# Kernel tuning notes

Hardware: AMD Instinct MI355X
Metric: run time of the kernel (lower is better)

Reference implementation:

```python
import jax, jax.numpy as jnp
import numpy as np

# Static problem sizes (see shape_source)
B, SX, SY = 256, 256, 70          # graphs, encoder nodes/graph, decoder nodes/graph
F, EMB, H = 512, 256, 256          # f_size, emb_size, h_size
VOCAB = 256
E = 4 * B * SY                     # 71680 edges
N_SLT = 4                          # SltEdgeTypes
N_SRT = 8                          # len(SrtEdgeTypes)


def setup_inputs() -> dict:
    key = jax.random.key(0)
    ks = jax.random.split(key, 24)
    s = 0.02
    inp = {
        'x': jax.random.normal(ks[0], (B * SX, F), jnp.float32),
        'x_batch': jnp.repeat(jnp.arange(B, dtype=jnp.int64), SX),
        'tgt_y': jax.random.randint(ks[1], (B * SY,), 0, VOCAB, jnp.int64),
        'tgt_edge_index': jax.random.randint(ks[2], (2, E), 0, B * SY, jnp.int64),
        'tgt_edge_type': jax.random.randint(ks[3], (E,), 0, N_SLT, jnp.int64),
        'tgt_y_batch': jnp.repeat(jnp.arange(B, dtype=jnp.int64), SY),
        'embeds': jax.random.normal(ks[4], (VOCAB, EMB), jnp.float32) * s,
    }
    dims = [(EMB, H), (H, H), (H, EMB)]
    k = 5
    for l, (din, dout) in enumerate(dims, start=1):
        inp[f'W_in{l}'] = jax.random.normal(ks[k + 0], (din, dout), jnp.float32) * s
        inp[f'Wq{l}'] = jax.random.normal(ks[k + 1], (dout, F), jnp.float32) * s
        inp[f'Wv{l}'] = jax.random.normal(ks[k + 2], (F, dout), jnp.float32) * s
        inp[f'Ee{l}'] = jax.random.normal(ks[k + 3], (N_SLT, dout), jnp.float32) * s
        k += 4
    inp['lin_z_w'] = jax.random.normal(ks[k], (EMB, VOCAB), jnp.float32) * s
    inp['lin_z_b'] = jnp.zeros((VOCAB,), jnp.float32)
    inp['lin_g_w'] = jax.random.normal(ks[k + 1], (2 * EMB, N_SRT), jnp.float32) * s
    inp['lin_g_b'] = jnp.zeros((N_SRT,), jnp.float32)
    return inp


def gcn_dec_layer(x_b, y, src, tgt, etype, W_in, Wq, Wv, Ee):
    """Edge-type-conditioned message passing + cross-attention onto encoder x.
    x_b: [B,SX,F]; y: [Ny,din]. Returns ([Ny,dout], alpha [B,SY,SX])."""
    h = y @ W_in                                   # [Ny, dout]
    m = h[src] + Ee[etype]                         # gather + type embedding
    agg = jax.ops.segment_sum(m, tgt, num_segments=y.shape[0])
    q = (h @ Wq).reshape(B, SY, F)                 # query into encoder space
    logits = jnp.einsum('bqf,bkf->bqk', q, x_b) / jnp.sqrt(jnp.float32(F))
    alpha = jax.nn.softmax(logits, axis=-1)        # [B,SY,SX]
    ctx = jnp.einsum('bqk,bkf->bqf', alpha, x_b) @ Wv  # [B,SY,dout]
    out = jax.nn.relu(h + agg + ctx.reshape(h.shape[0], -1))
    return out, alpha


def reference(x, x_batch, tgt_y, tgt_edge_index, tgt_edge_type, tgt_y_batch,
              embeds, W_in1, Wq1, Wv1, Ee1, W_in2, Wq2, Wv2, Ee2,
              W_in3, Wq3, Wv3, Ee3, lin_z_w, lin_z_b, lin_g_w, lin_g_b):
    x_b = x.reshape(B, SX, F)
    src, tgt = tgt_edge_index[0], tgt_edge_index[1]
    y = embeds[tgt_y]                              # [Ny, EMB]
    y, a1 = gcn_dec_layer(x_b, y, src, tgt, tgt_edge_type, W_in1, Wq1, Wv1, Ee1)
    y, a2 = gcn_dec_layer(x_b, y, src, tgt, tgt_edge_type, W_in2, Wq2, Wv2, Ee2)
    y, a3 = gcn_dec_layer(x_b, y, src, tgt, tgt_edge_type, W_in3, Wq3, Wv3, Ee3)
    y_score = y @ lin_z_w + lin_z_b                # [Ny, VOCAB]
    ef = y[tgt_edge_index]                         # [2, E, EMB]
    ef = jnp.transpose(ef, (1, 0, 2)).reshape(E, 2 * EMB)
    y_edge_rel_score = ef @ lin_g_w + lin_g_b      # [E, N_SRT]
    return (y, y_score, y_edge_rel_score, a1, a2, a3)
```

## Files before the change

### kernel.cpp

```cpp
#include <hip/hip_runtime.h>
#include <cstddef>
#include <cstdint>

#define B_    256
#define SX_   256
#define SY_   70
#define F_    512
#define EMB_  256
#define NY_   (B_*SY_)
#define NE_   (4*B_*SY_)

typedef short s16x8 __attribute__((ext_vector_type(8)));
typedef float f32x4 __attribute__((ext_vector_type(4)));
typedef unsigned short us4 __attribute__((ext_vector_type(4)));
typedef unsigned short us8 __attribute__((ext_vector_type(8)));

__device__ __forceinline__ unsigned short f2bf(float f) {
    unsigned u = __builtin_bit_cast(unsigned, f);
    u += 0x7fffu + ((u >> 16) & 1u);
    return (unsigned short)(u >> 16);
}
__device__ __forceinline__ float bf2f(unsigned short b) {
    unsigned u = ((unsigned)b) << 16;
    return __builtin_bit_cast(float, u);
}

template<int EPI, int SWZ>
__global__ __launch_bounds__(256, 2)
void gemm_mfma(const unsigned short* __restrict__ A, int lda, long sAb,
               const unsigned short* __restrict__ Bt, int ldb, long sBb,
               float* __restrict__ Cf, int ldc, long sCfb,
               unsigned short* __restrict__ Cb, int ldcb, long sCbb,
               const float* __restrict__ aux1, long sAux,
               int M, int K, float scale, int nx, int ny)
{
    __shared__ unsigned short As[128 * 64];
    __shared__ unsigned short Bs[128 * 64];
    char* AsB = (char*)As;
    char* BsB = (char*)Bs;
    const int tid = threadIdx.x;
    int bxi, byi, z;
    if (SWZ) {
        const int nwg = gridDim.x;
        const int bid = blockIdx.x;
        const int wg = (bid & 7) * (nwg >> 3) + (bid >> 3);
        bxi = wg % nx;
        byi = (wg / nx) % ny;
        z   = wg / (nx * ny);
    } else {
        bxi = blockIdx.x; byi = blockIdx.y; z = blockIdx.z;
    }
    A  += (size_t)z * sAb;
    Bt += (size_t)z * sBb;
    const char* auxp = (const char*)aux1 + (size_t)z * sAux;
    const int bm = byi * 128, bn = bxi * 128;
    const int lane = tid & 63;
    const int w = tid >> 6, wr = w >> 1, wc = w & 1;
    const int l15 = lane & 15, lq = lane >> 4;

    f32x4 acc[4][4];
    const f32x4 z4 = {0.f, 0.f, 0.f, 0.f};
#pragma unroll
    for (int m = 0; m < 4; ++m)
#pragma unroll
        for (int n = 0; n < 4; ++n) acc[m][n] = z4;

    for (int k0 = 0; k0 < K; k0 += 64) {
#pragma unroll
        for (int i = 0; i < 4; ++i) {
            const int row = i * 32 + (tid >> 3);
            const int k8  = (tid & 7) ^ (row & 7);
            int ra = bm + row; ra = (ra < M) ? ra : (M - 1);
            const unsigned short* g = A + (size_t)ra * lda + k0 + k8 * 8;
            __builtin_amdgcn_global_load_lds(
                (const __attribute__((address_space(1))) unsigned int*)g,
                (__attribute__((address_space(3))) unsigned int*)(AsB + i * 4096 + tid * 16),
                16, 0, 0);
        }
#pragma unroll
        for (int i = 0; i < 4; ++i) {
            const int row = i * 32 + (tid >> 3);
            const int k8  = (tid & 7) ^ (row & 7);
            const unsigned short* g = Bt + (size_t)(bn + row) * ldb + k0 + k8 * 8;
            __builtin_amdgcn_global_load_lds(
                (const __attribute__((address_space(1))) unsigned int*)g,
                (__attribute__((address_space(3))) unsigned int*)(BsB + i * 4096 + tid * 16),
                16, 0, 0);
        }
        __syncthreads();
#pragma unroll
        for (int kk = 0; kk < 2; ++kk) {
            s16x8 af[4], bf[4];
#pragma unroll
            for (int m = 0; m < 4; ++m) {
                const int row = wr * 64 + m * 16 + l15;
                const int slot = (kk * 4 + lq) ^ (row & 7);
                af[m] = *(const s16x8*)(AsB + row * 128 + slot * 16);
            }
#pragma unroll
            for (int n = 0; n < 4; ++n) {
                const int col = wc * 64 + n * 16 + l15;
                const int slot = (kk * 4 + lq) ^ (col & 7);
                bf[n] = *(const s16x8*)(BsB + col * 128 + slot * 16);
            }
#pragma unroll
            for (int m = 0; m < 4; ++m)
#pragma unroll
                for (int n = 0; n < 4; ++n)
                    acc[m][n] = __builtin_amdgcn_mfma_f32_16x16x32_bf16(
                        af[m], bf[n], acc[m][n], 0, 0, 0);
        }
        __syncthreads();
    }

    float* cf = Cf ? Cf + (size_t)z * sCfb : nullptr;
    unsigned short* cb = Cb ? Cb + (size_t)z * sCbb : nullptr;
#pragma unroll
    for (int m = 0; m < 4; ++m) {
#pragma unroll
        for (int n = 0; n < 4; ++n) {
            const int col = bn + wc * 64 + n * 16 + l15;
            f32x4 v = acc[m][n];
#pragma unroll
            for (int r = 0; r < 4; ++r) {
                const int gr = bm + wr * 64 + m * 16 + lq * 4 + r;
                if (gr >= M) continue;
                float o = v[r] * scale;
                if (EPI == 4) o += ((const float*)auxp)[col];
                if (EPI == 7) {
                    if (col < 256) cb[(size_t)gr * ldcb + col] = f2bf(o);
                    else ((unsigned short*)cf)[(size_t)gr * 512 + (col - 256)] = f2bf(o);
                } else {
                    if (cf) cf[(size_t)gr * ldc + col] = o;
                    if (cb) cb[(size_t)gr * ldcb + col] = f2bf(o);
                }
            }
        }
    }
}

template<int LAST>
__global__ __launch_bounds__(512, 1)
void attn_pv(const unsigned short* __restrict__ Q,
             const unsigned short* __restrict__ X,
             const unsigned short* __restrict__ XV,
             long sXVb,
             const unsigned short* __restrict__ aggb,
             const unsigned short* __restrict__ lzT,
             const float* __restrict__ lzb,
             float* __restrict__ Aout,
             unsigned short* __restrict__ Yb,
             float* __restrict__ Yf,
             float* __restrict__ Score,
             float scale)
{
    __shared__ unsigned short As[128 * 64];
    __shared__ unsigned short Bs[256 * 64];
    __shared__ unsigned short Al[128 * 256];
    __shared__ float red[4][2][64];
    char* AsB = (char*)As;
    char* BsB = (char*)Bs;
    char* AlB = (char*)Al;
    const int tid = threadIdx.x;
    const int z = blockIdx.x;
    const unsigned short* Qb  = Q + (size_t)z * SY_ * F_;
    const unsigned short* Xb  = X + (size_t)z * SX_ * F_;
    const unsigned short* xvb = XV + (size_t)z * sXVb;
    const int lane = tid & 63;
    const int w = tid >> 6, wr = w >> 2, wc = w & 3;
    const int l15 = lane & 15, lq = lane >> 4;

    f32x4 acc[4][4];
    const f32x4 z4 = {0.f, 0.f, 0.f, 0.f};
#pragma unroll
    for (int m = 0; m < 4; ++m)
#pragma unroll
        for (int n = 0; n < 4; ++n) acc[m][n] = z4;

    for (int k0 = 0; k0 < F_; k0 += 64) {
#pragma unroll
        for (int i = 0; i < 2; ++i) {
            const int row = i * 64 + (tid >> 3);
            const int k8  = (tid & 7) ^ (row & 7);
            const int ra = (row < SY_) ? row : (SY_ - 1);
            const unsigned short* g = Qb + (size_t)ra * F_ + k0 + k8 * 8;
            __builtin_amdgcn_global_load_lds(
                (const __attribute__((address_space(1))) unsigned int*)g,
                (__attribute__((address_space(3))) unsigned int*)(AsB + i * 8192 + tid * 16),
                16, 0, 0);
        }
#pragma unroll
        for (int i = 0; i < 4; ++i) {
            const int row = i * 64 + (tid >> 3);
            const int k8  = (tid & 7) ^ (row & 7);
            const unsigned short* g = Xb + (size_t)row * F_ + k0 + k8 * 8;
            __builtin_amdgcn_global_load_lds(
                (const __attribute__((address_space(1))) unsigned int*)g,
                (__attribute__((address_space(3))) unsigned int*)(BsB + i * 8192 + tid * 16),
                16, 0, 0);
        }
        __syncthreads();
#pragma unroll
        for (int kk = 0; kk < 2; ++kk) {
            s16x8 af[4], bf[4];
#pragma unroll
            for (int m = 0; m < 4; ++m) {
                const int row = wr * 64 + m * 16 + l15;
                const int slot = (kk * 4 + lq) ^ (row & 7);
                af[m] = *(const s16x8*)(AsB + row * 128 + slot * 16);
            }
#pragma unroll
            for (int n = 0; n < 4; ++n) {
                const int col = wc * 64 + n * 16 + l15;
                const int slot = (kk * 4 + lq) ^ (col & 7);
                bf[n] = *(const s16x8*)(BsB + col * 128 + slot * 16);
            }
#pragma unroll
            for (int m = 0; m < 4; ++m)
#pragma unroll
                for (int n = 0; n < 4; ++n)
                    acc[m][n] = __builtin_amdgcn_mfma_f32_16x16x32_bf16(
                        af[m], bf[n], acc[m][n], 0, 0, 0);
        }
        __syncthreads();
    }

#pragma unroll
    for (int m = 0; m < 4; ++m)
#pragma unroll
        for (int n = 0; n < 4; ++n)
#pragma unroll
            for (int r = 0; r < 4; ++r) acc[m][n][r] *= scale;

    float rmax[4][4];
#pragma unroll
    for (int m = 0; m < 4; ++m)
#pragma unroll
        for (int r = 0; r < 4; ++r) {
            float mx = acc[m][0][r];
#pragma unroll
            for (int n = 1; n < 4; ++n) mx = fmaxf(mx, acc[m][n][r]);
            mx = fmaxf(mx, __shfl_xor(mx, 1));
            mx = fmaxf(mx, __shfl_xor(mx, 2));
            mx = fmaxf(mx, __shfl_xor(mx, 4));
            mx = fmaxf(mx, __shfl_xor(mx, 8));
            rmax[m][r] = mx;
        }
    if (l15 == 0) {
#pragma unroll
        for (int m = 0; m < 4; ++m)
#pragma unroll
            for (int r = 0; r < 4; ++r)
                red[wc][wr][m * 16 + lq * 4 + r] = rmax[m][r];
    }
    __syncthreads();
    float rtot[4][4];
#pragma unroll
    for (int m = 0; m < 4; ++m)
#pragma unroll
        for (int r = 0; r < 4; ++r) {
            const int lr = m * 16 + lq * 4 + r;
            rtot[m][r] = fmaxf(fmaxf(red[0][wr][lr], red[1][wr][lr]),
                               fmaxf(red[2][wr][lr], red[3][wr][lr]));
        }
    __syncthreads();
    float rsum[4][4];
#pragma unroll
    for (int m = 0; m < 4; ++m)
#pragma unroll
        for (int r = 0; r < 4; ++r) {
            float s = 0.f;
#pragma unroll
            for (int n = 0; n < 4; ++n) {
                float e = __expf(acc[m][n][r] - rtot[m][r]);
                acc[m][n][r] = e;
                s += e;
            }
            s += __shfl_xor(s, 1);
            s += __shfl_xor(s, 2);
            s += __shfl_xor(s, 4);
            s += __shfl_xor(s, 8);
            rsum[m][r] = s;
        }
    if (l15 == 0) {
#pragma unroll
        for (int m = 0; m < 4; ++m)
#pragma unroll
            for (int r = 0; r < 4; ++r)
                red[wc][wr][m * 16 + lq * 4 + r] = rsum[m][r];
    }
    __syncthreads();
    float* ao = Aout + (size_t)z * SY_ * SX_;
#pragma unroll
    for (int m = 0; m < 4; ++m)
#pragma unroll
        for (int r = 0; r < 4; ++r) {
            const int lr = m * 16 + lq * 4 + r;
            const int row = wr * 64 + lr;
            const float inv = 1.0f / (red[0][wr][lr] + red[1][wr][lr] +
                                      red[2][wr][lr] + red[3][wr][lr]);
#pragma unroll
            for (int n = 0; n < 4; ++n) {
                const int col = wc * 64 + n * 16 + l15;
                const float o = acc[m][n][r] * inv;
                if (row < SY_) ao[(size_t)row * SX_ + col] = o;
                *(unsigned short*)(AlB + row * 512 +
                    (((col >> 3) ^ (row & 7)) << 4) + ((col & 7) << 1)) = f2bf(o);
            }
        }
    __syncthreads();

    f32x4 oac[4][4];
#pragma unroll
    for (int m = 0; m < 4; ++m)
#pragma unroll
        for (int n = 0; n < 4; ++n) oac[m][n] = z4;

    for (int ks = 0; ks < 4; ++ks) {
        const int k0 = ks * 64;
#pragma unroll
        for (int i = 0; i < 4; ++i) {
            const int row = i * 64 + (tid >> 3);
            const int k8  = (tid & 7) ^ (row & 7);
            const unsigned short* g = xvb + (size_t)row * 256 + k0 + k8 * 8;
            __builtin_amdgcn_global_load_lds(
                (const __attribute__((address_space(1))) unsigned int*)g,
                (__attribute__((address_space(3))) unsigned int*)(BsB + i * 8192 + tid * 16),
                16, 0, 0);
        }
        __syncthreads();
#pragma unroll
        for (int kk = 0; kk < 2; ++kk) {
            s16x8 af[4], bf[4];
#pragma unroll
            for (int m = 0; m < 4; ++m) {
                const int row = wr * 64 + m * 16 + l15;
                const int chunk = (k0 >> 3) + kk * 4 + lq;
                af[m] = *(const s16x8*)(AlB + row * 512 + ((chunk ^ (row & 7)) << 4));
            }
#pragma unroll
            for (int n = 0; n < 4; ++n) {
                const int col = wc * 64 + n * 16 + l15;
                const int slot = (kk * 4 + lq) ^ (col & 7);
                bf[n] = *(const s16x8*)(BsB + col * 128 + slot * 16);
            }
#pragma unroll
            for (int m = 0; m < 4; ++m)
#pragma unroll
                for (int n = 0; n < 4; ++n)
                    oac[m][n] = __builtin_amdgcn_mfma_f32_16x16x32_bf16(
                        af[m], bf[n], oac[m][n], 0, 0, 0);
        }
        __syncthreads();
    }

#pragma unroll
    for (int m = 0; m < 4; ++m)
#pragma unroll
        for (int n = 0; n < 4; ++n) {
            const int col = wc * 64 + n * 16 + l15;
            f32x4 v = oac[m][n];
#pragma unroll
            for (int r = 0; r < 4; ++r) {
                const int row = wr * 64 + m * 16 + lq * 4 + r;
                if (row >= SY_) continue;
                const size_t node = (size_t)z * SY_ + row;
                float o = v[r] + bf2f(aggb[node * 256 + col]);
                o = fmaxf(o, 0.f);
                const unsigned short ob = f2bf(o);
                Yb[node * 256 + col] = ob;
                if (Yf) Yf[node * 256 + col] = o;
                if (LAST)
                    *(unsigned short*)(AlB + row * 512 +
                        (((col >> 3) ^ (row & 7)) << 4) + ((col & 7) << 1)) = ob;
            }
        }

    if (LAST) {
        __syncthreads();
#pragma unroll
        for (int m = 0; m < 4; ++m)
#pragma unroll
            for (int n = 0; n < 4; ++n) oac[m][n] = z4;
        for (int ks = 0; ks < 4; ++ks) {
            const int k0 = ks * 64;
#pragma unroll
            for (int i = 0; i < 4; ++i) {
                const int row = i * 64 + (tid >> 3);
                const int k8  = (tid & 7) ^ (row & 7);
                const unsigned short* g = lzT + (size_t)row * 256 + k0 + k8 * 8;
                __builtin_amdgcn_global_load_lds(
                    (const __attribute__((address_space(1))) unsigned int*)g,
                    (__attribute__((address_space(3))) unsigned int*)(BsB + i * 8192 + tid * 16),
                    16, 0, 0);
            }
            __syncthreads();
#pragma unroll
            for (int kk = 0; kk < 2; ++kk) {
                s16x8 af[4], bf[4];
#pragma unroll
                for (int m = 0; m < 4; ++m) {
                    const int row = wr * 64 + m * 16 + l15;
                    const int chunk = (k0 >> 3) + kk * 4 + lq;
                    af[m] = *(const s16x8*)(AlB + row * 512 + ((chunk ^ (row & 7)) << 4));
                }
#pragma unroll
                for (int n = 0; n < 4; ++n) {
                    const int col = wc * 64 + n * 16 + l15;
                    const int slot = (kk * 4 + lq) ^ (col & 7);
                    bf[n] = *(const s16x8*)(BsB + col * 128 + slot * 16);
                }
#pragma unroll
                for (int m = 0; m < 4; ++m)
#pragma unroll
                    for (int n = 0; n < 4; ++n)
                        oac[m][n] = __builtin_amdgcn_mfma_f32_16x16x32_bf16(
                            af[m], bf[n], oac[m][n], 0, 0, 0);
            }
            __syncthreads();
        }
#pragma unroll
        for (int m = 0; m < 4; ++m)
#pragma unroll
            for (int n = 0; n < 4; ++n) {
                const int col = wc * 64 + n * 16 + l15;
                f32x4 v = oac[m][n];
#pragma unroll
                for (int r = 0; r < 4; ++r) {
                    const int row = wr * 64 + m * 16 + lq * 4 + r;
                    if (row >= SY_) continue;
                    Score[((size_t)z * SY_ + row) * 256 + col] = v[r] + lzb[col];
                }
            }
    }
}

__global__ __launch_bounds__(256)
void conv_x(const float* __restrict__ in, unsigned short* __restrict__ out, int n8)
{
    for (int i = blockIdx.x * 256 + threadIdx.x; i < n8; i += 2048 * 256) {
        float4 a = ((const float4*)in)[i * 2];
        float4 b = ((const float4*)in)[i * 2 + 1];
        us8 o = { f2bf(a.x), f2bf(a.y), f2bf(a.z), f2bf(a.w),
                  f2bf(b.x), f2bf(b.y), f2bf(b.z), f2bf(b.w) };
        ((us8*)out)[i] = o;
    }
}

struct WAll {
    const float* src[10];
    unsigned short* dst[10];
    int R[10];
    int C[10];
};

__global__ __launch_bounds__(256)
void conv_wT_all(WAll d)
{
    const int z = blockIdx.z;
    const int R = d.R[z], C = d.C[z];
    const int c0 = blockIdx.x * 64, r0 = blockIdx.y * 64;
    if (c0 >= C || r0 >= R) return;
    const float* in = d.src[z];
    unsigned short* outT = d.dst[z];
    __shared__ unsigned short t[64][65];
    const int r = threadIdx.x >> 4, cq = (threadIdx.x & 15) << 2;
#pragma unroll
    for (int i = 0; i < 4; ++i) {
        const int rr = r + i * 16;
        float4 v = *(const float4*)(in + (size_t)(r0 + rr) * C + c0 + cq);
        t[rr][cq + 0] = f2bf(v.x); t[rr][cq + 1] = f2bf(v.y);
        t[rr][cq + 2] = f2bf(v.z); t[rr][cq + 3] = f2bf(v.w);
    }
    __syncthreads();
    const int c = threadIdx.x >> 2, sq = (threadIdx.x & 3) << 4;
    us8 o0, o1;
#pragma unroll
    for (int i = 0; i < 8; ++i) { o0[i] = t[sq + i][c]; o1[i] = t[sq + 8 + i][c]; }
    *(us8*)(outT + (size_t)(c0 + c) * R + r0 + sq) = o0;
    *(us8*)(outT + (size_t)(c0 + c) * R + r0 + sq + 8) = o1;
}

__global__ __launch_bounds__(256)
void gather_embed(const float* __restrict__ embeds, const int* __restrict__ tgt_y,
                  unsigned short* __restrict__ yb)
{
    const int i = blockIdx.x * 8 + (threadIdx.x >> 5);
    const int c8 = (threadIdx.x & 31) * 8;
    const int v = tgt_y[i];
    const float* p = embeds + (size_t)v * 256 + c8;
    float4 a = *(const float4*)p;
    float4 b = *(const float4*)(p + 4);
    us8 o = { f2bf(a.x), f2bf(a.y), f2bf(a.z), f2bf(a.w),
              f2bf(b.x), f2bf(b.y), f2bf(b.z), f2bf(b.w) };
    *(us8*)(yb + (size_t)i * 256 + c8) = o;
}

__global__ __launch_bounds__(256)
void edge_deg(const int* __restrict__ tgt, int* __restrict__ deg)
{
    const int e = blockIdx.x * 256 + threadIdx.x;
    if (e < NE_) atomicAdd(&deg[tgt[e]], 1);
}

__global__ __launch_bounds__(1024)
void scan_off(const int* __restrict__ deg, int* __restrict__ off, int* __restrict__ cursor)
{
    __shared__ int ls[1024];
    const int t = threadIdx.x;
    const int base = t * 18;
    int local[18];
    int s = 0;
#pragma unroll
    for (int i = 0; i < 18; ++i) {
        const int idx = base + i;
        const int v = (idx < NY_) ? deg[idx] : 0;
        local[i] = s; s += v;
    }
    ls[t] = s;
    __syncthreads();
    for (int d = 1; d < 1024; d <<= 1) {
        int v = (t >= d) ? ls[t - d] : 0;
        __syncthreads();
        ls[t] += v;
        __syncthreads();
    }
    const int excl = (t == 0) ? 0 : ls[t - 1];
#pragma unroll
    for (int i = 0; i < 18; ++i) {
        const int idx = base + i;
        if (idx < NY_) {
            const int o = excl + local[i];
            off[idx] = o; cursor[idx] = o;
        }
    }
    if (t == 1023) off[NY_] = ls[1023];
}

__global__ __launch_bounds__(256)
void edge_fill(const int* __restrict__ tgt, int* __restrict__ cursor,
               int* __restrict__ elist)
{
    const int e = blockIdx.x * 256 + threadIdx.x;
    if (e >= NE_) return;
    const int pos = atomicAdd(&cursor[tgt[e]], 1);
    elist[pos] = e;
}

__global__ __launch_bounds__(256)
void node_agg(const unsigned short* __restrict__ hb,
              const float* __restrict__ Ee,
              const int* __restrict__ src, const int* __restrict__ etype,
              const int* __restrict__ off, const int* __restrict__ elist,
              unsigned short* __restrict__ aggb)
{
    const int nid  = blockIdx.x * 4 + (threadIdx.x >> 6);
    const int lane = threadIdx.x & 63;
    const int c = lane * 4;
    const int k0 = off[nid], k1 = off[nid + 1];
    us4 sv = *(const us4*)(hb + (size_t)nid * 256 + c);
    float4 acc;
    acc.x = bf2f(sv[0]); acc.y = bf2f(sv[1]);
    acc.z = bf2f(sv[2]); acc.w = bf2f(sv[3]);
    int cnt0 = 0, cnt1 = 0, cnt2 = 0, cnt3 = 0;
    for (int k = k0; k < k1; ++k) {
        const int e = elist[k];
        const int sfrom = src[e];
        const int ty = etype[e];
        us4 hv = *(const us4*)(hb + (size_t)sfrom * 256 + c);
        acc.x += bf2f(hv[0]); acc.y += bf2f(hv[1]);
        acc.z += bf2f(hv[2]); acc.w += bf2f(hv[3]);
        cnt0 += (ty == 0); cnt1 += (ty == 1); cnt2 += (ty == 2); cnt3 += (ty == 3);
    }
    float4 e0 = *(const float4*)(Ee + c);
    float4 e1 = *(const float4*)(Ee + 256 + c);
    float4 e2 = *(const float4*)(Ee + 512 + c);
    float4 e3 = *(const float4*)(Ee + 768 + c);
    acc.x += cnt0 * e0.x + cnt1 * e1.x + cnt2 * e2.x + cnt3 * e3.x;
    acc.y += cnt0 * e0.y + cnt1 * e1.y + cnt2 * e2.y + cnt3 * e3.y;
    acc.z += cnt0 * e0.z + cnt1 * e1.z + cnt2 * e2.z + cnt3 * e3.z;
    acc.w += cnt0 * e0.w + cnt1 * e1.w + cnt2 * e2.w + cnt3 * e3.w;
    us4 o = { f2bf(acc.x), f2bf(acc.y), f2bf(acc.z), f2bf(acc.w) };
    *(us4*)(aggb + (size_t)nid * 256 + c) = o;
}

__global__ __launch_bounds__(256)
void edge_w(const float* __restrict__ y, const float* __restrict__ W,
            float* __restrict__ Y12)
{
    __shared__ float Ws[4096];
    __shared__ float ys[16][260];
    const int tid = threadIdx.x;
#pragma unroll
    for (int i = 0; i < 4; ++i)
        ((float4*)Ws)[i * 256 + tid] = ((const float4*)W)[i * 256 + tid];
    const int r = tid >> 4, seg = tid & 15;
    const int r0 = blockIdx.x * 16;
#pragma unroll
    for (int i = 0; i < 4; ++i) {
        const int c4 = seg + i * 16;
        *(float4*)&ys[r][c4 * 4] = *(const float4*)(y + (size_t)(r0 + r) * 256 + c4 * 4);
    }
    __syncthreads();
    const int j = tid & 15;
    const int row = tid >> 4;
    const float* Wcol = Ws + ((j < 8) ? j : (2048 + j - 8));
    float acc = 0.f;
#pragma unroll 4
    for (int c = 0; c < 256; ++c) acc = fmaf(ys[row][c], Wcol[c * 8], acc);
    Y12[(size_t)(r0 + row) * 16 + j] = acc;
}

__global__ __launch_bounds__(256)
void edge_gather(const float* __restrict__ Y12, const int* __restrict__ src,
                 const int* __restrict__ tgt, const float* __restrict__ bias,
                 float* __restrict__ esc)
{
    const int e = blockIdx.x * 256 + threadIdx.x;
    if (e >= NE_) return;
    const float* a = Y12 + (size_t)src[e] * 16;
    const float* b = Y12 + (size_t)tgt[e] * 16 + 8;
    float4 a0 = ((const float4*)a)[0], a1 = ((const float4*)a)[1];
    float4 b0 = ((const float4*)b)[0], b1 = ((const float4*)b)[1];
    float4 c0 = ((const float4*)bias)[0], c1 = ((const float4*)bias)[1];
    float4 o0, o1;
    o0.x = a0.x + b0.x + c0.x; o0.y = a0.y + b0.y + c0.y;
    o0.z = a0.z + b0.z + c0.z; o0.w = a0.w + b0.w + c0.w;
    o1.x = a1.x + b1.x + c1.x; o1.y = a1.y + b1.y + c1.y;
    o1.z = a1.z + b1.z + c1.z; o1.w = a1.w + b1.w + c1.w;
    ((float4*)(esc + (size_t)e * 8))[0] = o0;
    ((float4*)(esc + (size_t)e * 8))[1] = o1;
}

extern "C" void kernel_launch(void* const* d_in, const int* in_sizes, int n_in,
                              void* d_out, int out_size, void* d_ws, size_t ws_size,
                              hipStream_t stream)
{
    const float* x       = (const float*)d_in[0];
    const int*   tgt_y   = (const int*)d_in[2];
    const int*   eidx    = (const int*)d_in[3];
    const int*   etype   = (const int*)d_in[4];
    const float* embeds  = (const float*)d_in[6];
    const float* W_in[3] = {(const float*)d_in[7],  (const float*)d_in[11], (const float*)d_in[15]};
    const float* Wq[3]   = {(const float*)d_in[8],  (const float*)d_in[12], (const float*)d_in[16]};
    const float* Wv[3]   = {(const float*)d_in[9],  (const float*)d_in[13], (const float*)d_in[17]};
    const float* Ee[3]   = {(const float*)d_in[10], (const float*)d_in[14], (const float*)d_in[18]};
    const float* lin_z_w = (const float*)d_in[19];
    const float* lin_z_b = (const float*)d_in[20];
    const float* lin_g_w = (const float*)d_in[21];
    const float* lin_g_b = (const float*)d_in[22];
    const int* src = eidx;
    const int* tgt = eidx + NE_;

    float* out = (float*)d_out;
    float* y_final = out;
    float* score   = out + 4587520;
    float* esc     = out + 9175040;
    float* aout[3] = {out + 9748480, out + 14336000, out + 18923520};

    char* wsb = (char*)d_ws;
    unsigned short* xb     = (unsigned short*)(wsb + 0);
    unsigned short* xvTall = (unsigned short*)(wsb + 67108864);
    unsigned short* hb     = (unsigned short*)(wsb + 167772160);
    unsigned short* aggb   = (unsigned short*)(wsb + 176947200);
    unsigned short* qb     = (unsigned short*)(wsb + 186122240);
    unsigned short* yb     = (unsigned short*)(wsb + 204472320);
    char* wt = wsb + 213647360;
    unsigned short* wcatT[3], *wqT[3], *wvT[3];
    for (int l = 0; l < 3; ++l) {
        wcatT[l] = (unsigned short*)(wt + l * 393216);
        wqT[l]   = (unsigned short*)(wt + 1179648 + l * 262144);
        wvT[l]   = (unsigned short*)(wt + 1966080 + l * 262144);
    }
    unsigned short* lzT = (unsigned short*)(wt + 2752512);
    char* extra = wsb + 216530944;
    float* Y12    = (float*)extra;
    int*   deg    = (int*)(extra + 1146880);
    int*   off    = (int*)(extra + 1218560);
    int*   cursor = (int*)(extra + 1290244);
    int*   elist  = (int*)(extra + 1361924);

    hipMemsetAsync(deg, 0, NY_ * sizeof(int), stream);
    edge_deg<<<280, 256, 0, stream>>>(tgt, deg);
    scan_off<<<1, 1024, 0, stream>>>(deg, off, cursor);
    edge_fill<<<280, 256, 0, stream>>>(tgt, cursor, elist);

    conv_x<<<2048, 256, 0, stream>>>(x, xb, 4194304);
    WAll wd;
    for (int l = 0; l < 3; ++l) {
        wd.src[l]     = W_in[l]; wd.dst[l]     = wcatT[l]; wd.R[l]     = 256; wd.C[l]     = 256;
        wd.src[3 + l] = Wq[l];   wd.dst[3 + l] = wqT[l];   wd.R[3 + l] = 256; wd.C[3 + l] = 512;
        wd.src[6 + l] = Wv[l];   wd.dst[6 + l] = wvT[l];   wd.R[6 + l] = 512; wd.C[6 + l] = 256;
    }
    wd.src[9] = lin_z_w; wd.dst[9] = lzT; wd.R[9] = 256; wd.C[9] = 256;
    conv_wT_all<<<dim3(8, 8, 10), 256, 0, stream>>>(wd);
    gather_embed<<<2240, 256, 0, stream>>>(embeds, tgt_y, yb);

    gemm_mfma<0, 0><<<dim3(2, 4, 3), 256, 0, stream>>>(
        wqT[0], 256, 131072L,  wcatT[0], 256, 196608L,
        nullptr, 0, 0,  wcatT[0] + 65536, 256, 196608L,
        nullptr, 0, 512, 256, 1.f, 0, 0);

    gemm_mfma<0, 1><<<3072, 256, 0, stream>>>(
        wvT[0], 512, 0,  xb, 512, (long)SX_ * F_,
        nullptr, 0, 0,  xvTall, 256, 768L * 256,
        nullptr, 0, 768, 512, 1.f, 2, 6);

    const float qscale = 0.044194173824159216f;
    for (int l = 0; l < 3; ++l) {
        gemm_mfma<7, 0><<<dim3(6, 140, 1), 256, 0, stream>>>(
            yb, 256, 0,  wcatT[l], 256, 0,
            (float*)qb, 512, 0,  hb, 256, 0,
            nullptr, 0, NY_, 256, 1.f, 0, 0);
        node_agg<<<4480, 256, 0, stream>>>(hb, Ee[l], src, etype, off, elist, aggb);
        if (l < 2) {
            attn_pv<0><<<256, 512, 0, stream>>>(
                qb, xb, xvTall + (size_t)l * 65536, 768L * 256,
                aggb, nullptr, nullptr,
                aout[l], yb, nullptr, nullptr, qscale);
        } else {
            attn_pv<1><<<256, 512, 0, stream>>>(
                qb, xb, xvTall + (size_t)l * 65536, 768L * 256,
                aggb, lzT, lin_z_b,
                aout[l], yb, y_final, score, qscale);
        }
    }
    edge_w<<<1120, 256, 0, stream>>>(y_final, lin_g_w, Y12);
    edge_gather<<<280, 256, 0, stream>>>(Y12, src, tgt, lin_g_b, esc);
}
```

Baseline: 444.7 us.

## Fuse CSR build into one kernel, merge embed gather, fold edge_w into attention

Collapses the memset, degree count, scan and fill into a single one-block kernel using LDS atomics. Merges the embedding gather into the x conversion launch. Moves the per-node edge-weight projection into the last attention kernel, reading the final y from LDS. This cuts launch count and a y reload, but the single-block CSR build serialises 71680 edges on one CU, and the fused epilogue runs scalar FMA loops at the tail of attn_pv.

```diff
diff --git a/kernel.cpp b/kernel.cpp
--- a/kernel.cpp
+++ b/kernel.cpp
@@ -148,6 +148,8 @@
              const unsigned short* __restrict__ aggb,
              const unsigned short* __restrict__ lzT,
              const float* __restrict__ lzb,
+             const float* __restrict__ gw,
+             float* __restrict__ Y12g,
              float* __restrict__ Aout,
              unsigned short* __restrict__ Yb,
              float* __restrict__ Yf,
@@ -432,18 +434,49 @@
                     Score[((size_t)z * SY_ + row) * 256 + col] = v[r] + lzb[col];
                 }
             }
+
+        __syncthreads();
+        float* Ws = (float*)BsB;
+        for (int i = tid; i < 1024; i += 512)
+            ((float4*)Ws)[i] = ((const float4*)gw)[i];
+        __syncthreads();
+        for (int t = tid; t < 1120; t += 512) {
+            const int row = t >> 4, j = t & 15;
+            const float* Wcol = Ws + ((j < 8) ? j : (2048 + j - 8));
+            float a2 = 0.f;
+            for (int c = 0; c < 256; ++c) {
+                const float yv = bf2f(*(const unsigned short*)(AlB + row * 512 +
+                    (((c >> 3) ^ (row & 7)) << 4) + ((c & 7) << 1)));
+                a2 = fmaf(yv, Wcol[c * 8], a2);
+            }
+            Y12g[((size_t)z * SY_ + row) * 16 + j] = a2;
+        }
     }
 }
 
 __global__ __launch_bounds__(256)
-void conv_x(const float* __restrict__ in, unsigned short* __restrict__ out, int n8)
+void conv_x_embed(const float* __restrict__ in, unsigned short* __restrict__ out,
+                  int n8, const float* __restrict__ embeds,
+                  const int* __restrict__ tgt_y, unsigned short* __restrict__ yb)
 {
-    for (int i = blockIdx.x * 256 + threadIdx.x; i < n8; i += 2048 * 256) {
-        float4 a = ((const float4*)in)[i * 2];
-        float4 b = ((const float4*)in)[i * 2 + 1];
+    if (blockIdx.x < 2048) {
+        for (int i = blockIdx.x * 256 + threadIdx.x; i < n8; i += 2048 * 256) {
+            float4 a = ((const float4*)in)[i * 2];
+            float4 b = ((const float4*)in)[i * 2 + 1];
+            us8 o = { f2bf(a.x), f2bf(a.y), f2bf(a.z), f2bf(a.w),
+                      f2bf(b.x), f2bf(b.y), f2bf(b.z), f2bf(b.w) };
+            ((us8*)out)[i] = o;
+        }
+    } else {
+        const int i = (blockIdx.x - 2048) * 8 + (threadIdx.x >> 5);
+        const int c8 = (threadIdx.x & 31) * 8;
+        const int v = tgt_y[i];
+        const float* p = embeds + (size_t)v * 256 + c8;
+        float4 a = *(const float4*)p;
+        float4 b = *(const float4*)(p + 4);
         us8 o = { f2bf(a.x), f2bf(a.y), f2bf(a.z), f2bf(a.w),
                   f2bf(b.x), f2bf(b.y), f2bf(b.z), f2bf(b.w) };
-        ((us8*)out)[i] = o;
+        *(us8*)(yb + (size_t)i * 256 + c8) = o;
     }
 }
 
@@ -481,40 +514,24 @@
     *(us8*)(outT + (size_t)(c0 + c) * R + r0 + sq + 8) = o1;
 }
 
-__global__ __launch_bounds__(256)
-void gather_embed(const float* __restrict__ embeds, const int* __restrict__ tgt_y,
-                  unsigned short* __restrict__ yb)
+__global__ __launch_bounds__(1024)
+void build_csr(const int* __restrict__ tgt, int* __restrict__ off,
+               int* __restrict__ elist)
 {
-    const int i = blockIdx.x * 8 + (threadIdx.x >> 5);
-    const int c8 = (threadIdx.x & 31) * 8;
-    const int v = tgt_y[i];
-    const float* p = embeds + (size_t)v * 256 + c8;
-    float4 a = *(const float4*)p;
-    float4 b = *(const float4*)(p + 4);
-    us8 o = { f2bf(a.x), f2bf(a.y), f2bf(a.z), f2bf(a.w),
-              f2bf(b.x), f2bf(b.y), f2bf(b.z), f2bf(b.w) };
-    *(us8*)(yb + (size_t)i * 256 + c8) = o;
-}
-
-__global__ __launch_bounds__(256)
-void edge_deg(const int* __restrict__ tgt, int* __restrict__ deg)
-{
-    const int e = blockIdx.x * 256 + threadIdx.x;
-    if (e < NE_) atomicAdd(&deg[tgt[e]], 1);
-}
-
-__global__ __launch_bounds__(1024)
-void scan_off(const int* __restrict__ deg, int* __restrict__ off, int* __restrict__ cursor)
-{
+    __shared__ int ldeg[NY_];
     __shared__ int ls[1024];
     const int t = threadIdx.x;
+    for (int i = t; i < NY_; i += 1024) ldeg[i] = 0;
+    __syncthreads();
+    for (int e = t; e < NE_; e += 1024) atomicAdd(&ldeg[tgt[e]], 1);
+    __syncthreads();
     const int base = t * 18;
     int local[18];
     int s = 0;
 #pragma unroll
     for (int i = 0; i < 18; ++i) {
         const int idx = base + i;
-        const int v = (idx < NY_) ? deg[idx] : 0;
+        const int v = (idx < NY_) ? ldeg[idx] : 0;
         local[i] = s; s += v;
     }
     ls[t] = s;
@@ -531,20 +548,16 @@
         const int idx = base + i;
         if (idx < NY_) {
             const int o = excl + local[i];
-            off[idx] = o; cursor[idx] = o;
+            off[idx] = o;
+            ldeg[idx] = o;
         }
     }
     if (t == 1023) off[NY_] = ls[1023];
-}
-
-__global__ __launch_bounds__(256)
-void edge_fill(const int* __restrict__ tgt, int* __restrict__ cursor,
-               int* __restrict__ elist)
-{
-    const int e = blockIdx.x * 256 + threadIdx.x;
-    if (e >= NE_) return;
-    const int pos = atomicAdd(&cursor[tgt[e]], 1);
-    elist[pos] = e;
+    __syncthreads();
+    for (int e = t; e < NE_; e += 1024) {
+        const int pos = atomicAdd(&ldeg[tgt[e]], 1);
+        elist[pos] = e;
+    }
 }
 
 __global__ __launch_bounds__(256)
@@ -585,33 +598,6 @@
 }
 
 __global__ __launch_bounds__(256)
-void edge_w(const float* __restrict__ y, const float* __restrict__ W,
-            float* __restrict__ Y12)
-{
-    __shared__ float Ws[4096];
-    __shared__ float ys[16][260];
-    const int tid = threadIdx.x;
-#pragma unroll
-    for (int i = 0; i < 4; ++i)
-        ((float4*)Ws)[i * 256 + tid] = ((const float4*)W)[i * 256 + tid];
-    const int r = tid >> 4, seg = tid & 15;
-    const int r0 = blockIdx.x * 16;
-#pragma unroll
-    for (int i = 0; i < 4; ++i) {
-        const int c4 = seg + i * 16;
-        *(float4*)&ys[r][c4 * 4] = *(const float4*)(y + (size_t)(r0 + r) * 256 + c4 * 4);
-    }
-    __syncthreads();
-    const int j = tid & 15;
-    const int row = tid >> 4;
-    const float* Wcol = Ws + ((j < 8) ? j : (2048 + j - 8));
-    float acc = 0.f;
-#pragma unroll 4
-    for (int c = 0; c < 256; ++c) acc = fmaf(ys[row][c], Wcol[c * 8], acc);
-    Y12[(size_t)(r0 + row) * 16 + j] = acc;
-}
-
-__global__ __launch_bounds__(256)
 void edge_gather(const float* __restrict__ Y12, const int* __restrict__ src,
                  const int* __restrict__ tgt, const float* __restrict__ bias,
                  float* __restrict__ esc)
@@ -675,17 +661,12 @@
     unsigned short* lzT = (unsigned short*)(wt + 2752512);
     char* extra = wsb + 216530944;
     float* Y12    = (float*)extra;
-    int*   deg    = (int*)(extra + 1146880);
-    int*   off    = (int*)(extra + 1218560);
-    int*   cursor = (int*)(extra + 1290244);
-    int*   elist  = (int*)(extra + 1361924);
-
-    hipMemsetAsync(deg, 0, NY_ * sizeof(int), stream);
-    edge_deg<<<280, 256, 0, stream>>>(tgt, deg);
-    scan_off<<<1, 1024, 0, stream>>>(deg, off, cursor);
-    edge_fill<<<280, 256, 0, stream>>>(tgt, cursor, elist);
-
-    conv_x<<<2048, 256, 0, stream>>>(x, xb, 4194304);
+    int*   off    = (int*)(extra + 1146880);
+    int*   elist  = (int*)(extra + 1218568);
+
+    build_csr<<<1, 1024, 0, stream>>>(tgt, off, elist);
+
+    conv_x_embed<<<4288, 256, 0, stream>>>(x, xb, 4194304, embeds, tgt_y, yb);
     WAll wd;
     for (int l = 0; l < 3; ++l) {
         wd.src[l]     = W_in[l]; wd.dst[l]     = wcatT[l]; wd.R[l]     = 256; wd.C[l]     = 256;
@@ -694,7 +675,6 @@
     }
     wd.src[9] = lin_z_w; wd.dst[9] = lzT; wd.R[9] = 256; wd.C[9] = 256;
     conv_wT_all<<<dim3(8, 8, 10), 256, 0, stream>>>(wd);
-    gather_embed<<<2240, 256, 0, stream>>>(embeds, tgt_y, yb);
 
     gemm_mfma<0, 0><<<dim3(2, 4, 3), 256, 0, stream>>>(
         wqT[0], 256, 131072L,  wcatT[0], 256, 196608L,
@@ -716,15 +696,14 @@
         if (l < 2) {
             attn_pv<0><<<256, 512, 0, stream>>>(
                 qb, xb, xvTall + (size_t)l * 65536, 768L * 256,
-                aggb, nullptr, nullptr,
+                aggb, nullptr, nullptr, nullptr, nullptr,
                 aout[l], yb, nullptr, nullptr, qscale);
         } else {
             attn_pv<1><<<256, 512, 0, stream>>>(
                 qb, xb, xvTall + (size_t)l * 65536, 768L * 256,
-                aggb, lzT, lin_z_b,
+                aggb, lzT, lin_z_b, lin_g_w, Y12,
                 aout[l], yb, y_final, score, qscale);
         }
     }
-    edge_w<<<1120, 256, 0, stream>>>(y_final, lin_g_w, Y12);
     edge_gather<<<280, 256, 0, stream>>>(Y12, src, tgt, lin_g_b, esc);
 }
```

Measured after the change: 468.5 us. 1.05x slower.
